# Kernel tuning notes

Measured on AMD Instinct MI355X. Metric: run time of the kernel, lower is better.

The kernel has to match this reference:

```python
import jax, jax.numpy as jnp
import numpy as np

T = 4            # timesteps (init arg T)
K = 8            # num_thresholds
B = 64           # batch per timestep (x.shape[0] == T*B)


def setup_inputs() -> dict:
    key = jax.random.key(0)
    kx, = jax.random.split(key, 1)
    x = jax.random.normal(kx, (T * B, 128, 32, 32), dtype=jnp.float32)
    thresh = jnp.asarray(1.0, dtype=jnp.float32)  # scalar learnable threshold
    return {"x": x, "thresh": thresh}


def reference(x, thresh):
    # thre_shaped: thresh / 2**k, shaped [K, 1,1,1,1] to broadcast over mem[None] = [1,B,C,H,W]
    thre = (thresh / (2.0 ** jnp.arange(K, dtype=x.dtype))).reshape((K,) + (1,) * x.ndim)
    thr75 = thre * 0.75

    xt = x.reshape((T, x.shape[0] // T) + x.shape[1:])  # expand: [T, B, C, H, W]

    def step(mem, xc):
        mem = mem + xc
        # which thresholds the membrane exceeds (thresholds are decreasing in k)
        pos = (mem[None] >= thr75).astype(x.dtype)           # [K, B, C, H, W]
        pos_true = pos.at[1:].add(-pos[:-1])                 # first (largest) crossed threshold only
        spike = jnp.sum(thre * pos_true, axis=0)             # [B, C, H, W]
        return mem - spike, spike

    mem0 = jnp.zeros_like(xt[0])
    _, spikes = jax.lax.scan(step, mem0, xt)                 # spikes: [T, B, C, H, W]
    return spikes.reshape(x.shape)                            # merge: [T*B, C, H, W]
```

## Files before the change

kernel.cpp:

```cpp
#include <hip/hip_runtime.h>


constexpr int T_STEPS = 4;
constexpr int BLOCK = 256;
constexpr int GRID = 1024;

typedef float v4f __attribute__((ext_vector_type(4)));

__device__ __forceinline__ void load4(v4f dst[T_STEPS], const v4f* __restrict__ xv,
                                      size_t n, size_t j) {
#pragma unroll
    for (int t = 0; t < T_STEPS; ++t) dst[t] = xv[(size_t)t * n + j];
}

__device__ __forceinline__ float spike_of(float mem, int b75_0, int b75_7, int bth0) {
    int u = __float_as_int(mem);
    int d = (int)((unsigned)b75_0 - (unsigned)u);
    int k = (int)((unsigned)d + 0x7fffffu) >> 23;
    k = k > 0 ? k : 0;
    int sb = bth0 - (k << 23);
    return (u >= b75_7) ? __int_as_float(sb) : 0.0f;
}

__device__ __forceinline__ void process(const v4f a[T_STEPS], v4f* __restrict__ ov,
                                        size_t n, size_t j,
                                        int b75_0, int b75_7, int bth0) {
    v4f sp[T_STEPS];
#pragma unroll
    for (int e = 0; e < 4; ++e) {
        float mem = a[0][e];
        float s0 = spike_of(mem, b75_0, b75_7, bth0);
        sp[0][e] = s0;
        mem = mem - s0 + a[1][e];
        float s1 = spike_of(mem, b75_0, b75_7, bth0);
        sp[1][e] = s1;
        mem = mem - s1 + a[2][e];
        float s2 = spike_of(mem, b75_0, b75_7, bth0);
        sp[2][e] = s2;
        mem = mem - s2 + a[3][e];
        sp[3][e] = spike_of(mem, b75_0, b75_7, bth0);
    }
#pragma unroll
    for (int t = 0; t < T_STEPS; ++t)
        __builtin_nontemporal_store(sp[t], &ov[(size_t)t * n + j]);
}

__global__ __launch_bounds__(BLOCK) void snn_mth_kernel(
    const float* __restrict__ x,
    const float* __restrict__ p_thresh,
    float* __restrict__ out,
    int s4)
{
    const float thresh = *p_thresh;
    const int bth0  = __float_as_int(thresh);
    const int b75_0 = __float_as_int(0.75f * thresh);
    const int b75_7 = b75_0 - 7 * 0x800000;

    const v4f* __restrict__ xv = reinterpret_cast<const v4f*>(x);
    v4f* __restrict__ ov = reinterpret_cast<v4f*>(out);

    const size_t n = (size_t)s4;
    const size_t stride = (size_t)GRID * BLOCK;

    size_t jA = (size_t)blockIdx.x * BLOCK + threadIdx.x;
    v4f A[T_STEPS], B[T_STEPS];
    bool actA = jA < n;
    if (actA) load4(A, xv, n, jA);

    while (actA) {
        size_t jB = jA + stride;
        bool actB = jB < n;
        if (actB) load4(B, xv, n, jB);
        process(A, ov, n, jA, b75_0, b75_7, bth0);

        size_t jA2 = jB + stride;
        actA = jA2 < n;
        if (actA) load4(A, xv, n, jA2);
        if (!actB) break;
        process(B, ov, n, jB, b75_0, b75_7, bth0);
        jA = jA2;
    }
}

extern "C" void kernel_launch(void* const* d_in, const int* in_sizes, int n_in,
                              void* d_out, int out_size, void* d_ws, size_t ws_size,
                              hipStream_t stream) {
    const float* x = (const float*)d_in[0];
    const float* p_thresh = (const float*)d_in[1];
    float* out = (float*)d_out;

    const int total = in_sizes[0];
    const int S = total / T_STEPS;
    const int s4 = S >> 2;

    snn_mth_kernel<<<GRID, BLOCK, 0, stream>>>(x, p_thresh, out, s4);
}
```

Before: 246.7 us.

## Replace grid-stride loop with one-chunk-per-thread launch and XCD-contiguous block remap

Drops the persistent 1024-block grid-stride loop with software double-buffering and launches one block per 256 float4 columns, each thread handling a single chunk across all timesteps. Block indices are remapped so that blocks landing on the same XCD (round-robin by blockIdx mod 8) cover one contiguous segment of the input. This aims for better DRAM/L2 locality per XCD and removes loop overhead, at the cost of launching many more blocks and losing the explicit load/compute overlap.

```diff
diff --git a/kernel.cpp b/kernel.cpp
--- a/kernel.cpp
+++ b/kernel.cpp
@@ -3,15 +3,9 @@
 
 constexpr int T_STEPS = 4;
 constexpr int BLOCK = 256;
-constexpr int GRID = 1024;
+constexpr int NXCD = 8;
 
 typedef float v4f __attribute__((ext_vector_type(4)));
-
-__device__ __forceinline__ void load4(v4f dst[T_STEPS], const v4f* __restrict__ xv,
-                                      size_t n, size_t j) {
-#pragma unroll
-    for (int t = 0; t < T_STEPS; ++t) dst[t] = xv[(size_t)t * n + j];
-}
 
 __device__ __forceinline__ float spike_of(float mem, int b75_0, int b75_7, int bth0) {
     int u = __float_as_int(mem);
@@ -20,29 +14,6 @@
     k = k > 0 ? k : 0;
     int sb = bth0 - (k << 23);
     return (u >= b75_7) ? __int_as_float(sb) : 0.0f;
-}
-
-__device__ __forceinline__ void process(const v4f a[T_STEPS], v4f* __restrict__ ov,
-                                        size_t n, size_t j,
-                                        int b75_0, int b75_7, int bth0) {
-    v4f sp[T_STEPS];
-#pragma unroll
-    for (int e = 0; e < 4; ++e) {
-        float mem = a[0][e];
-        float s0 = spike_of(mem, b75_0, b75_7, bth0);
-        sp[0][e] = s0;
-        mem = mem - s0 + a[1][e];
-        float s1 = spike_of(mem, b75_0, b75_7, bth0);
-        sp[1][e] = s1;
-        mem = mem - s1 + a[2][e];
-        float s2 = spike_of(mem, b75_0, b75_7, bth0);
-        sp[2][e] = s2;
-        mem = mem - s2 + a[3][e];
-        sp[3][e] = spike_of(mem, b75_0, b75_7, bth0);
-    }
-#pragma unroll
-    for (int t = 0; t < T_STEPS; ++t)
-        __builtin_nontemporal_store(sp[t], &ov[(size_t)t * n + j]);
 }
 
 __global__ __launch_bounds__(BLOCK) void snn_mth_kernel(
@@ -59,27 +30,47 @@
     const v4f* __restrict__ xv = reinterpret_cast<const v4f*>(x);
     v4f* __restrict__ ov = reinterpret_cast<v4f*>(out);
 
+    const int seg_cols   = s4 / (NXCD * BLOCK) * BLOCK;
+    const int seg_blocks = seg_cols / BLOCK;
+    const int main_blocks = seg_blocks * NXCD;
+
+    const int b = blockIdx.x;
+    size_t j;
+    if (b < main_blocks) {
+        const int xcd  = b % NXCD;
+        const int slot = b / NXCD;
+        j = (size_t)xcd * seg_cols + (size_t)slot * BLOCK + threadIdx.x;
+    } else {
+        j = (size_t)NXCD * seg_cols + (size_t)(b - main_blocks) * BLOCK + threadIdx.x;
+        if (j >= (size_t)s4) return;
+    }
+
     const size_t n = (size_t)s4;
-    const size_t stride = (size_t)GRID * BLOCK;
 
-    size_t jA = (size_t)blockIdx.x * BLOCK + threadIdx.x;
-    v4f A[T_STEPS], B[T_STEPS];
-    bool actA = jA < n;
-    if (actA) load4(A, xv, n, jA);
+    v4f xc[T_STEPS];
+#pragma unroll
+    for (int t = 0; t < T_STEPS; ++t)
+        xc[t] = xv[(size_t)t * n + j];
 
-    while (actA) {
-        size_t jB = jA + stride;
-        bool actB = jB < n;
-        if (actB) load4(B, xv, n, jB);
-        process(A, ov, n, jA, b75_0, b75_7, bth0);
+    v4f sp[T_STEPS];
+#pragma unroll
+    for (int e = 0; e < 4; ++e) {
+        float mem = xc[0][e];
+        float s0 = spike_of(mem, b75_0, b75_7, bth0);
+        sp[0][e] = s0;
+        mem = mem - s0 + xc[1][e];
+        float s1 = spike_of(mem, b75_0, b75_7, bth0);
+        sp[1][e] = s1;
+        mem = mem - s1 + xc[2][e];
+        float s2 = spike_of(mem, b75_0, b75_7, bth0);
+        sp[2][e] = s2;
+        mem = mem - s2 + xc[3][e];
+        sp[3][e] = spike_of(mem, b75_0, b75_7, bth0);
+    }
 
-        size_t jA2 = jB + stride;
-        actA = jA2 < n;
-        if (actA) load4(A, xv, n, jA2);
-        if (!actB) break;
-        process(B, ov, n, jB, b75_0, b75_7, bth0);
-        jA = jA2;
-    }
+#pragma unroll
+    for (int t = 0; t < T_STEPS; ++t)
+        __builtin_nontemporal_store(sp[t], &ov[(size_t)t * n + j]);
 }
 
 extern "C" void kernel_launch(void* const* d_in, const int* in_sizes, int n_in,
@@ -93,5 +84,6 @@
     const int S = total / T_STEPS;
     const int s4 = S >> 2;
 
-    snn_mth_kernel<<<GRID, BLOCK, 0, stream>>>(x, p_thresh, out, s4);
+    const int grid = (s4 + BLOCK - 1) / BLOCK;
+    snn_mth_kernel<<<grid, BLOCK, 0, stream>>>(x, p_thresh, out, s4);
 }
```

Result: faster. 234.0 us (-5.1%).
